# Kernel optimization log

Measured on AMD Instinct MI355X. Metric: run time of the kernel, lower is better.

Reference implementation:

```python
import jax, jax.numpy as jnp
import numpy as np

N = 50000
E = 800000
DIN = 128
DOUT = 128
T = 4  # number of edge types: onset, consecutive, during, rest


def setup_inputs() -> dict:
    key = jax.random.key(0)
    ks = jax.random.split(key, 12)
    s = 1.0 / np.sqrt(DIN)
    inp = {
        "x": jax.random.normal(ks[0], (N, DIN), dtype=jnp.float32),
        "edge_index": jax.random.randint(ks[1], (2, E), 0, N, dtype=jnp.int32),
        "edge_type": jax.random.randint(ks[2], (E,), 0, T, dtype=jnp.int32),
        # stacked per-etype parameters of ResGatedGraphConv
        "Wk": jax.random.uniform(ks[3], (T, DIN, DOUT), jnp.float32, -s, s),
        "bk": jax.random.uniform(ks[4], (T, DOUT), jnp.float32, -s, s),
        "Wq": jax.random.uniform(ks[5], (T, DIN, DOUT), jnp.float32, -s, s),
        "bq": jax.random.uniform(ks[6], (T, DOUT), jnp.float32, -s, s),
        "Wv": jax.random.uniform(ks[7], (T, DIN, DOUT), jnp.float32, -s, s),
        "bv": jax.random.uniform(ks[8], (T, DOUT), jnp.float32, -s, s),
        "Ws": jax.random.uniform(ks[9], (T, DIN, DOUT), jnp.float32, -s, s),
        "b": jax.random.uniform(ks[10], (T, DOUT), jnp.float32, -s, s),
    }
    return inp


def reference(x, edge_index, edge_type, Wk, bk, Wq, bq, Wv, bv, Ws, b):
    # PyG ResGatedGraphConv per edge type t, with edges masked to that type:
    #   out_i = sum_{j->i, type==t} sigmoid(k_i + q_j) * v_j + Ws_t x_i + b_t
    # followed by mean over edge types ('mean' reduction).
    src = edge_index[0]  # j (message source)
    dst = edge_index[1]  # i (message target)
    n = x.shape[0]
    outs = []
    for t in range(T):
        k = x @ Wk[t] + bk[t]  # [N, DOUT]
        q = x @ Wq[t] + bq[t]
        v = x @ Wv[t] + bv[t]
        eta = jax.nn.sigmoid(k[dst] + q[src])        # [E, DOUT]
        msg = eta * v[src]                            # [E, DOUT]
        msg = jnp.where((edge_type == t)[:, None], msg, 0.0)
        agg = jax.ops.segment_sum(msg, dst, num_segments=n)
        outs.append(agg + x @ Ws[t] + b[t])
    return jnp.mean(jnp.stack(outs, axis=0), axis=0)  # [N, DOUT]
```

## Files before the change

kernel.cpp:

```cpp
#include <hip/hip_runtime.h>

typedef unsigned short u16;
typedef unsigned int u32;
typedef __attribute__((ext_vector_type(8))) short bf16x8;
typedef __attribute__((ext_vector_type(4))) float f32x4;
typedef __attribute__((ext_vector_type(2))) float f32x2;
typedef __attribute__((ext_vector_type(8))) u16 u16x8;
typedef __attribute__((ext_vector_type(4))) u16 u16x4;
typedef __attribute__((ext_vector_type(2))) u16 u16x2;
typedef __attribute__((ext_vector_type(2))) u32 u32x2;

#define DIM 128
#define AS1C(p) ((const __attribute__((address_space(1))) void*)(p))
#define AS3P(p) ((__attribute__((address_space(3))) void*)(p))

__device__ __forceinline__ u32 f2bf(float f){
  u32 x = __float_as_uint(f);
  return (x + 0x7fffu + ((x >> 16) & 1u)) >> 16;
}
__device__ __forceinline__ float bf2f(u16 u){
  return __uint_as_float(((u32)u) << 16);
}

__global__ __launch_bounds__(256) void prep_kernel(
    const float* __restrict__ x, u16* __restrict__ xb,
    const float* __restrict__ Wk, const float* __restrict__ bk,
    const float* __restrict__ Wq, const float* __restrict__ bq,
    const float* __restrict__ Wv, const float* __restrict__ bv,
    const float* __restrict__ Ws, const float* __restrict__ bb,
    u16* __restrict__ WcatT, float* __restrict__ biascat,
    int* __restrict__ cnt, int T, int N, int rows){
  int id = blockIdx.x * 256 + threadIdx.x;
  int total_w = (3 * T + 1) * DIM * DIM;
  int total_cast = rows * (DIM / 4);
  if (id >= total_w){
    int z = id - total_w;
    if (z < total_cast){
      int el = z * 4;
      int node = el >> 7;
      u32x2 pk;
      if (node < N){
        f32x4 v = *(const f32x4*)(x + el);
        pk.x = f2bf(v.x) | (f2bf(v.y) << 16);
        pk.y = f2bf(v.z) | (f2bf(v.w) << 16);
      } else { pk.x = 0u; pk.y = 0u; }
      *(u32x2*)(xb + el) = pk;
    } else {
      int z2 = z - total_cast;
      if (z2 < N) cnt[z2] = 0;
    }
    return;
  }
  int kk = id & (DIM - 1);
  int c  = id >> 7;
  int qvspan = 2 * T * DIM;
  float wv, bvv;
  if (c < qvspan){
    int t = c >> 8;
    int w = c & 255;
    int j = w >> 1;
    if ((w & 1) == 0){ wv = Wq[(t*DIM + kk)*DIM + j]; bvv = bq[t*DIM + j]; }
    else             { wv = Wv[(t*DIM + kk)*DIM + j]; bvv = bv[t*DIM + j]; }
  } else if (c < qvspan + T * DIM){
    int t = (c - qvspan) >> 7;
    int j = (c - qvspan) & (DIM - 1);
    wv = Wk[(t*DIM + kk)*DIM + j]; bvv = bk[t*DIM + j];
  } else {
    int j = c - 3 * T * DIM;
    float s = 0.f, sb = 0.f;
    for (int t = 0; t < T; ++t){ s += Ws[(t*DIM + kk)*DIM + j]; sb += bb[t*DIM + j]; }
    wv = s / (float)T; bvv = sb / (float)T;
  }
  WcatT[(size_t)c * DIM + kk] = (u16)f2bf(wv);
  if (kk == 0) biascat[c] = bvv;
}

__global__ __launch_bounds__(256) void hist_kernel(const int* __restrict__ dst,
                                                   int* __restrict__ cnt,
                                                   int* __restrict__ rank, int E){
  int e = blockIdx.x * 256 + threadIdx.x;
  if (e < E) rank[e] = atomicAdd(&cnt[dst[e]], 1);
}

__global__ __launch_bounds__(256) void scan1_kernel(const int* __restrict__ cnt,
                                                    int* __restrict__ offs,
                                                    int* __restrict__ bsum, int n){
  __shared__ int wsum[4];
  const int tid = threadIdx.x;
  const int lane = tid & 63, wave = tid >> 6;
  const int base = blockIdx.x * 2048 + tid * 8;
  int v[8]; int tot = 0;
#pragma unroll
  for (int j = 0; j < 8; ++j){
    int idx = base + j;
    int val = (idx < n) ? cnt[idx] : 0;
    v[j] = val; tot += val;
  }
  int incl = tot;
#pragma unroll
  for (int d = 1; d < 64; d <<= 1){
    int u = __shfl_up(incl, d, 64);
    if (lane >= d) incl += u;
  }
  if (lane == 63) wsum[wave] = incl;
  __syncthreads();
  int wbase = 0;
#pragma unroll
  for (int w = 0; w < 4; ++w) if (w < wave) wbase += wsum[w];
  int excl = wbase + incl - tot;
  if (tid == 255) bsum[blockIdx.x] = wbase + incl;
#pragma unroll
  for (int j = 0; j < 8; ++j){
    int idx = base + j;
    if (idx < n) offs[idx] = excl;
    excl += v[j];
  }
}

__global__ __launch_bounds__(64) void scan2_kernel(const int* __restrict__ bsum,
                                                   int* __restrict__ boffs, int nb){
  int lane = threadIdx.x;
  int v = (lane < nb) ? bsum[lane] : 0;
  int incl = v;
#pragma unroll
  for (int d = 1; d < 64; d <<= 1){
    int u = __shfl_up(incl, d, 64);
    if (lane >= d) incl += u;
  }
  if (lane < nb) boffs[lane] = incl - v;
}

__global__ __launch_bounds__(256) void scatter_kernel(const int* __restrict__ src,
                                                      const int* __restrict__ dst,
                                                      const int* __restrict__ et,
                                                      const int* __restrict__ offs,
                                                      const int* __restrict__ boffs,
                                                      const int* __restrict__ rank,
                                                      int* __restrict__ packed, int E){
  int e = blockIdx.x * 256 + threadIdx.x;
  if (e >= E) return;
  int d = dst[e];
  int pos = offs[d] + boffs[d >> 11] + rank[e];
  packed[pos] = (src[e] << 2) | (et[e] & 3);
}

__global__ __launch_bounds__(256, 4) void gemm_kernel(const u16* __restrict__ xb,
                                                      const u16* __restrict__ WcatT,
                                                      const float* __restrict__ biascat,
                                                      u16* __restrict__ Y,
                                                      int N, int ncol, int NB, int mtiles){
  __shared__ u16 wt[DIM * DIM];
  int bid = blockIdx.x;
  int body = NB * (mtiles & ~7);
  int mt, nt;
  if (bid < body){
    int g = bid >> 3, r = bid & 7;
    int a = g / NB;
    mt = a * 8 + r;
    nt = g - a * NB;
  } else {
    int z = bid - body;
    mt = (mtiles & ~7) + z / NB;
    nt = z % NB;
  }
  const int m0 = mt * 128;
  const int n0 = nt * 128;
  const int tid  = threadIdx.x;
  const int wave = tid >> 6;
  const int lane = tid & 63;
  const int l15  = lane & 15;
  const int quad = lane >> 4;
  const int wrow = wave * 32;

  const u16* xrow0 = xb + (size_t)(m0 + wrow + l15) * DIM + quad * 8;
  const u16* xrow1 = xrow0 + 16 * DIM;

  bf16x8 bcur[2], bnxt[2];
  bcur[0] = *(const bf16x8*)(xrow0 + 0);
  bcur[1] = *(const bf16x8*)(xrow1 + 0);
  bnxt[0] = *(const bf16x8*)(xrow0 + 32);
  bnxt[1] = *(const bf16x8*)(xrow1 + 32);

#pragma unroll
  for (int it = 0; it < 8; ++it){
    int s  = it * 256 + tid;
    int r  = s >> 4;
    int p  = s & 15;
    int lb = p ^ (r & 7);
    int lbase = (it * 256 + wave * 64) * 8;
    __builtin_amdgcn_global_load_lds(AS1C(WcatT + (size_t)(n0 + r) * DIM + lb * 8),
                                     AS3P(wt + lbase), 16, 0, 0);
  }
  __syncthreads();

  f32x4 acc[2][8];
#pragma unroll
  for (int m = 0; m < 2; ++m)
#pragma unroll
    for (int f = 0; f < 8; ++f)
      acc[m][f] = (f32x4){0.f, 0.f, 0.f, 0.f};

#pragma unroll
  for (int ks = 0; ks < 4; ++ks){
    bf16x8 b0 = bcur[0], b1 = bcur[1];
    if (ks < 3){
      bcur[0] = bnxt[0]; bcur[1] = bnxt[1];
      if (ks < 2){
        bnxt[0] = *(const bf16x8*)(xrow0 + (ks + 2) * 32);
        bnxt[1] = *(const bf16x8*)(xrow1 + (ks + 2) * 32);
      }
    }
    const int pb8 = (((ks * 4 + quad) ^ (l15 & 7)) * 8);
#pragma unroll
    for (int f = 0; f < 8; ++f){
      bf16x8 afr = *(const bf16x8*)&wt[(f * 16 + l15) * DIM + pb8];
      acc[0][f] = __builtin_amdgcn_mfma_f32_16x16x32_bf16(afr, b0, acc[0][f], 0, 0, 0);
      acc[1][f] = __builtin_amdgcn_mfma_f32_16x16x32_bf16(afr, b1, acc[1][f], 0, 0, 0);
    }
  }

#pragma unroll
  for (int m = 0; m < 2; ++m){
    int node = m0 + wrow + m * 16 + l15;
    if (node >= N) continue;
    size_t rowbase = (size_t)node * ncol;
#pragma unroll
    for (int f = 0; f < 8; ++f){
      int feat = n0 + f * 16 + quad * 4;
      f32x4 b4 = *(const f32x4*)&biascat[feat];
      f32x4 v  = acc[m][f];
      u32 lo = f2bf(v.x + b4.x) | (f2bf(v.y + b4.y) << 16);
      u32 hi = f2bf(v.z + b4.z) | (f2bf(v.w + b4.w) << 16);
      u32x2 pk = {lo, hi};
      *(u32x2*)&Y[rowbase + feat] = pk;
    }
  }
}

__global__ __launch_bounds__(256) void agg_kernel(const u16* __restrict__ Y,
                                                  const int* __restrict__ offs,
                                                  const int* __restrict__ boffs,
                                                  const int* __restrict__ packed,
                                                  float* __restrict__ out,
                                                  int N, int E, float invT, int ncol){
  const int wave = threadIdx.x >> 6;
  const int lane = threadIdx.x & 63;
  const int half = lane >> 5;
  const int l32  = lane & 31;
  const int node = blockIdx.x * 8 + wave * 2 + half;
  const bool valid = node < N;
  const int nc = valid ? node : N - 1;

  const int kqoff = 1024;
  const int soff  = 1536;
  const u16* yr = Y + (size_t)nc * ncol;
  const int c4 = l32 * 4;

  u16x4 kw[4];
#pragma unroll
  for (int t = 0; t < 4; ++t)
    kw[t] = *(const u16x4*)(yr + kqoff + t * DIM + c4);
  u16x4 sw = *(const u16x4*)(yr + soff + c4);

  int e0 = 0, e1 = 0;
  if (valid){
    e0 = offs[nc] + boffs[nc >> 11];
    e1 = (nc == N - 1) ? E : (offs[nc + 1] + boffs[(nc + 1) >> 11]);
  }

  f32x4 acc = {0.f, 0.f, 0.f, 0.f};
  int e = e0;
  for (; e + 8 <= e1; e += 8){
    int p[8];
#pragma unroll
    for (int j = 0; j < 8; ++j) p[j] = packed[e + j];
    u16x8 a[8];
#pragma unroll
    for (int j = 0; j < 8; ++j)
      a[j] = *(const u16x8*)(Y + (size_t)(p[j] >> 2) * ncol + (p[j] & 3) * 256 + l32 * 8);
#pragma unroll
    for (int j = 0; j < 8; ++j){
      int t = p[j] & 3;
      u16x4 kwt = (t == 0) ? kw[0] : (t == 1) ? kw[1] : (t == 2) ? kw[2] : kw[3];
      acc.x += bf2f(a[j].s1) * __builtin_amdgcn_rcpf(1.f + __expf(-(bf2f(kwt.x) + bf2f(a[j].s0))));
      acc.y += bf2f(a[j].s3) * __builtin_amdgcn_rcpf(1.f + __expf(-(bf2f(kwt.y) + bf2f(a[j].s2))));
      acc.z += bf2f(a[j].s5) * __builtin_amdgcn_rcpf(1.f + __expf(-(bf2f(kwt.z) + bf2f(a[j].s4))));
      acc.w += bf2f(a[j].s7) * __builtin_amdgcn_rcpf(1.f + __expf(-(bf2f(kwt.w) + bf2f(a[j].s6))));
    }
  }
  for (; e < e1; ++e){
    int p = packed[e];
    int t = p & 3;
    u16x8 a = *(const u16x8*)(Y + (size_t)(p >> 2) * ncol + t * 256 + l32 * 8);
    u16x4 kwt = (t == 0) ? kw[0] : (t == 1) ? kw[1] : (t == 2) ? kw[2] : kw[3];
    acc.x += bf2f(a.s1) * __builtin_amdgcn_rcpf(1.f + __expf(-(bf2f(kwt.x) + bf2f(a.s0))));
    acc.y += bf2f(a.s3) * __builtin_amdgcn_rcpf(1.f + __expf(-(bf2f(kwt.y) + bf2f(a.s2))));
    acc.z += bf2f(a.s5) * __builtin_amdgcn_rcpf(1.f + __expf(-(bf2f(kwt.z) + bf2f(a.s4))));
    acc.w += bf2f(a.s7) * __builtin_amdgcn_rcpf(1.f + __expf(-(bf2f(kwt.w) + bf2f(a.s6))));
  }
  if (valid){
    f32x4 o = { invT * acc.x + bf2f(sw.x), invT * acc.y + bf2f(sw.y),
                invT * acc.z + bf2f(sw.z), invT * acc.w + bf2f(sw.w) };
    *(f32x4*)&out[(size_t)node * DIM + c4] = o;
  }
}

extern "C" void kernel_launch(void* const* d_in, const int* in_sizes, int n_in,
                              void* d_out, int out_size, void* d_ws, size_t ws_size,
                              hipStream_t stream){
  const float* x  = (const float*)d_in[0];
  const int*   ei = (const int*)d_in[1];
  const int*   et = (const int*)d_in[2];
  const float* Wk = (const float*)d_in[3];
  const float* bk = (const float*)d_in[4];
  const float* Wq = (const float*)d_in[5];
  const float* bq = (const float*)d_in[6];
  const float* Wv = (const float*)d_in[7];
  const float* bv = (const float*)d_in[8];
  const float* Ws = (const float*)d_in[9];
  const float* bb = (const float*)d_in[10];
  float* out = (float*)d_out;

  const int N = in_sizes[0] / DIM;
  const int E = in_sizes[2];
  const int T = in_sizes[3] / (DIM * DIM);
  const int NB = 3 * T + 1;
  const int ncol = NB * DIM;
  const int mtiles = (N + 127) / 128;
  const int rows = mtiles * 128;
  const int nscan = (N + 2047) / 2048;

  char* ws = (char*)d_ws;
  size_t off = 0;
  auto alloc = [&](size_t bytes) -> char* {
    char* p = ws + off;
    off = (off + bytes + 255) & ~(size_t)255;
    return p;
  };
  u16*   xb      = (u16*)alloc((size_t)rows * DIM * 2);
  u16*   WcatT   = (u16*)alloc((size_t)ncol * DIM * 2);
  float* biascat = (float*)alloc((size_t)ncol * 4);
  u16*   Y       = (u16*)alloc((size_t)N * ncol * 2);
  int*   cnt     = (int*)alloc((size_t)N * 4);
  int*   offs    = (int*)alloc((size_t)N * 4);
  int*   rank    = (int*)alloc((size_t)E * 4);
  int*   packed  = (int*)alloc((size_t)E * 4);
  int*   bsum    = (int*)alloc((size_t)nscan * 4);
  int*   boffs   = (int*)alloc((size_t)nscan * 4);
  (void)ws_size; (void)n_in; (void)out_size;

  const int* srcp = ei;
  const int* dstp = ei + E;

  int prep_total = NB * DIM * DIM + rows * (DIM / 4) + N;
  prep_kernel<<<(prep_total + 255) / 256, 256, 0, stream>>>(x, xb, Wk, bk, Wq, bq, Wv, bv,
                                                            Ws, bb, WcatT, biascat, cnt, T, N, rows);
  hist_kernel<<<(E + 255) / 256, 256, 0, stream>>>(dstp, cnt, rank, E);
  scan1_kernel<<<nscan, 256, 0, stream>>>(cnt, offs, bsum, N);
  scan2_kernel<<<1, 64, 0, stream>>>(bsum, boffs, nscan);
  scatter_kernel<<<(E + 255) / 256, 256, 0, stream>>>(srcp, dstp, et, offs, boffs, rank, packed, E);
  gemm_kernel<<<NB * mtiles, 256, 0, stream>>>(xb, WcatT, biascat, Y, N, ncol, NB, mtiles);
  agg_kernel<<<(N + 7) / 8, 256, 0, stream>>>(Y, offs, boffs, packed, out, N, E, 1.0f / (float)T, ncol);
}
```

Measured before the change: 306.1 us.

## Store q in fp8, repack Y rows, and fuse hist/scatter into prep and gemm

```diff
diff --git a/kernel.cpp b/kernel.cpp
--- a/kernel.cpp
+++ b/kernel.cpp
@@ -4,13 +4,15 @@
 typedef unsigned int u32;
 typedef __attribute__((ext_vector_type(8))) short bf16x8;
 typedef __attribute__((ext_vector_type(4))) float f32x4;
-typedef __attribute__((ext_vector_type(2))) float f32x2;
 typedef __attribute__((ext_vector_type(8))) u16 u16x8;
 typedef __attribute__((ext_vector_type(4))) u16 u16x4;
-typedef __attribute__((ext_vector_type(2))) u16 u16x2;
 typedef __attribute__((ext_vector_type(2))) u32 u32x2;
 
 #define DIM 128
+#define ROWB 2816
+#define QV_SPAN 384
+#define K_OFF 1536
+#define S_OFF 2560
 #define AS1C(p) ((const __attribute__((address_space(1))) void*)(p))
 #define AS3P(p) ((__attribute__((address_space(3))) void*)(p))
 
@@ -24,62 +26,51 @@
 
 __global__ __launch_bounds__(256) void prep_kernel(
     const float* __restrict__ x, u16* __restrict__ xb,
+    const int* __restrict__ dst, int* __restrict__ cnt, int* __restrict__ rank,
     const float* __restrict__ Wk, const float* __restrict__ bk,
     const float* __restrict__ Wq, const float* __restrict__ bq,
     const float* __restrict__ Wv, const float* __restrict__ bv,
     const float* __restrict__ Ws, const float* __restrict__ bb,
     u16* __restrict__ WcatT, float* __restrict__ biascat,
-    int* __restrict__ cnt, int T, int N, int rows){
+    int T, int N, int E, int rows){
   int id = blockIdx.x * 256 + threadIdx.x;
+  if (id < E){
+    rank[id] = atomicAdd(&cnt[dst[id]], 1);
+    return;
+  }
+  id -= E;
   int total_w = (3 * T + 1) * DIM * DIM;
+  if (id < total_w){
+    int kk = id & (DIM - 1);
+    int c  = id >> 7;
+    int nt = c >> 7;
+    int j  = c & (DIM - 1);
+    float wv, bvv;
+    if (nt < T)          { wv = Wq[(nt*DIM + kk)*DIM + j];      bvv = bq[nt*DIM + j]; }
+    else if (nt < 2*T)   { wv = Wv[((nt-T)*DIM + kk)*DIM + j];  bvv = bv[(nt-T)*DIM + j]; }
+    else if (nt < 3*T)   { wv = Wk[((nt-2*T)*DIM + kk)*DIM + j];bvv = bk[(nt-2*T)*DIM + j]; }
+    else {
+      float s = 0.f, sb = 0.f;
+      for (int t = 0; t < T; ++t){ s += Ws[(t*DIM + kk)*DIM + j]; sb += bb[t*DIM + j]; }
+      wv = s / (float)T; bvv = sb / (float)T;
+    }
+    WcatT[(size_t)c * DIM + kk] = (u16)f2bf(wv);
+    if (kk == 0) biascat[c] = bvv;
+    return;
+  }
+  id -= total_w;
   int total_cast = rows * (DIM / 4);
-  if (id >= total_w){
-    int z = id - total_w;
-    if (z < total_cast){
-      int el = z * 4;
-      int node = el >> 7;
-      u32x2 pk;
-      if (node < N){
-        f32x4 v = *(const f32x4*)(x + el);
-        pk.x = f2bf(v.x) | (f2bf(v.y) << 16);
-        pk.y = f2bf(v.z) | (f2bf(v.w) << 16);
-      } else { pk.x = 0u; pk.y = 0u; }
-      *(u32x2*)(xb + el) = pk;
-    } else {
-      int z2 = z - total_cast;
-      if (z2 < N) cnt[z2] = 0;
-    }
-    return;
-  }
-  int kk = id & (DIM - 1);
-  int c  = id >> 7;
-  int qvspan = 2 * T * DIM;
-  float wv, bvv;
-  if (c < qvspan){
-    int t = c >> 8;
-    int w = c & 255;
-    int j = w >> 1;
-    if ((w & 1) == 0){ wv = Wq[(t*DIM + kk)*DIM + j]; bvv = bq[t*DIM + j]; }
-    else             { wv = Wv[(t*DIM + kk)*DIM + j]; bvv = bv[t*DIM + j]; }
-  } else if (c < qvspan + T * DIM){
-    int t = (c - qvspan) >> 7;
-    int j = (c - qvspan) & (DIM - 1);
-    wv = Wk[(t*DIM + kk)*DIM + j]; bvv = bk[t*DIM + j];
-  } else {
-    int j = c - 3 * T * DIM;
-    float s = 0.f, sb = 0.f;
-    for (int t = 0; t < T; ++t){ s += Ws[(t*DIM + kk)*DIM + j]; sb += bb[t*DIM + j]; }
-    wv = s / (float)T; bvv = sb / (float)T;
-  }
-  WcatT[(size_t)c * DIM + kk] = (u16)f2bf(wv);
-  if (kk == 0) biascat[c] = bvv;
-}
-
-__global__ __launch_bounds__(256) void hist_kernel(const int* __restrict__ dst,
-                                                   int* __restrict__ cnt,
-                                                   int* __restrict__ rank, int E){
-  int e = blockIdx.x * 256 + threadIdx.x;
-  if (e < E) rank[e] = atomicAdd(&cnt[dst[e]], 1);
+  if (id < total_cast){
+    int el = id * 4;
+    int node = el >> 7;
+    u32x2 pk;
+    if (node < N){
+      f32x4 v = *(const f32x4*)(x + el);
+      pk.x = f2bf(v.x) | (f2bf(v.y) << 16);
+      pk.y = f2bf(v.z) | (f2bf(v.w) << 16);
+    } else { pk.x = 0u; pk.y = 0u; }
+    *(u32x2*)(xb + el) = pk;
+  }
 }
 
 __global__ __launch_bounds__(256) void scan1_kernel(const int* __restrict__ cnt,
@@ -130,27 +121,26 @@
   if (lane < nb) boffs[lane] = incl - v;
 }
 
-__global__ __launch_bounds__(256) void scatter_kernel(const int* __restrict__ src,
-                                                      const int* __restrict__ dst,
-                                                      const int* __restrict__ et,
-                                                      const int* __restrict__ offs,
-                                                      const int* __restrict__ boffs,
-                                                      const int* __restrict__ rank,
-                                                      int* __restrict__ packed, int E){
-  int e = blockIdx.x * 256 + threadIdx.x;
-  if (e >= E) return;
-  int d = dst[e];
-  int pos = offs[d] + boffs[d >> 11] + rank[e];
-  packed[pos] = (src[e] << 2) | (et[e] & 3);
-}
-
-__global__ __launch_bounds__(256, 4) void gemm_kernel(const u16* __restrict__ xb,
-                                                      const u16* __restrict__ WcatT,
-                                                      const float* __restrict__ biascat,
-                                                      u16* __restrict__ Y,
-                                                      int N, int ncol, int NB, int mtiles){
+__global__ __launch_bounds__(256, 4) void gemm_scatter_kernel(
+    const u16* __restrict__ xb, const u16* __restrict__ WcatT,
+    const float* __restrict__ biascat, char* __restrict__ Y,
+    const int* __restrict__ src, const int* __restrict__ dst,
+    const int* __restrict__ et, const int* __restrict__ offs,
+    const int* __restrict__ boffs, const int* __restrict__ rank,
+    int* __restrict__ packed,
+    int N, int E, int T, int NB, int mtiles, int nsc){
   __shared__ u16 wt[DIM * DIM];
   int bid = blockIdx.x;
+  if (bid < nsc){
+    int e = bid * 256 + threadIdx.x;
+    if (e < E){
+      int d = dst[e];
+      int pos = offs[d] + boffs[d >> 11] + rank[e];
+      packed[pos] = (src[e] << 2) | (et[e] & 3);
+    }
+    return;
+  }
+  bid -= nsc;
   int body = NB * (mtiles & ~7);
   int mt, nt;
   if (bid < body){
@@ -223,26 +213,37 @@
   for (int m = 0; m < 2; ++m){
     int node = m0 + wrow + m * 16 + l15;
     if (node >= N) continue;
-    size_t rowbase = (size_t)node * ncol;
+    char* rb = Y + (size_t)node * ROWB;
 #pragma unroll
     for (int f = 0; f < 8; ++f){
-      int feat = n0 + f * 16 + quad * 4;
-      f32x4 b4 = *(const f32x4*)&biascat[feat];
+      int feat = f * 16 + quad * 4;
+      f32x4 b4 = *(const f32x4*)&biascat[n0 + feat];
       f32x4 v  = acc[m][f];
-      u32 lo = f2bf(v.x + b4.x) | (f2bf(v.y + b4.y) << 16);
-      u32 hi = f2bf(v.z + b4.z) | (f2bf(v.w + b4.w) << 16);
-      u32x2 pk = {lo, hi};
-      *(u32x2*)&Y[rowbase + feat] = pk;
-    }
-  }
-}
-
-__global__ __launch_bounds__(256) void agg_kernel(const u16* __restrict__ Y,
+      float a0 = v.x + b4.x, a1 = v.y + b4.y, a2 = v.z + b4.z, a3 = v.w + b4.w;
+      if (nt < T){
+        u32 w = __builtin_amdgcn_cvt_pk_fp8_f32(a0, a1, 0, false);
+        w = __builtin_amdgcn_cvt_pk_fp8_f32(a2, a3, w, true);
+        *(u32*)(rb + nt * QV_SPAN + feat) = w;
+      } else {
+        u32 lo = f2bf(a0) | (f2bf(a1) << 16);
+        u32 hi = f2bf(a2) | (f2bf(a3) << 16);
+        u32x2 pk = {lo, hi};
+        int boff;
+        if (nt < 2*T)      boff = (nt - T) * QV_SPAN + 128;
+        else if (nt < 3*T) boff = K_OFF + (nt - 2*T) * 256;
+        else               boff = S_OFF;
+        *(u32x2*)(rb + boff + feat * 2) = pk;
+      }
+    }
+  }
+}
+
+__global__ __launch_bounds__(256) void agg_kernel(const char* __restrict__ Y,
                                                   const int* __restrict__ offs,
                                                   const int* __restrict__ boffs,
                                                   const int* __restrict__ packed,
                                                   float* __restrict__ out,
-                                                  int N, int E, float invT, int ncol){
+                                                  int N, int E, float invT){
   const int wave = threadIdx.x >> 6;
   const int lane = threadIdx.x & 63;
   const int half = lane >> 5;
@@ -251,16 +252,15 @@
   const bool valid = node < N;
   const int nc = valid ? node : N - 1;
 
-  const int kqoff = 1024;
-  const int soff  = 1536;
-  const u16* yr = Y + (size_t)nc * ncol;
-  const int c4 = l32 * 4;
-
-  u16x4 kw[4];
-#pragma unroll
-  for (int t = 0; t < 4; ++t)
-    kw[t] = *(const u16x4*)(yr + kqoff + t * DIM + c4);
-  u16x4 sw = *(const u16x4*)(yr + soff + c4);
+  const char* yr = Y + (size_t)nc * ROWB;
+
+  f32x4 kf[4];
+#pragma unroll
+  for (int t = 0; t < 4; ++t){
+    u16x4 kw = *(const u16x4*)(yr + K_OFF + t * 256 + l32 * 8);
+    kf[t] = (f32x4){ bf2f(kw.x), bf2f(kw.y), bf2f(kw.z), bf2f(kw.w) };
+  }
+  u16x4 sw = *(const u16x4*)(yr + S_OFF + l32 * 8);
 
   int e0 = 0, e1 = 0;
   if (valid){
@@ -274,34 +274,39 @@
     int p[8];
 #pragma unroll
     for (int j = 0; j < 8; ++j) p[j] = packed[e + j];
-    u16x8 a[8];
-#pragma unroll
-    for (int j = 0; j < 8; ++j)
-      a[j] = *(const u16x8*)(Y + (size_t)(p[j] >> 2) * ncol + (p[j] & 3) * 256 + l32 * 8);
+    u32 qw[8]; u16x4 vw[8];
+#pragma unroll
+    for (int j = 0; j < 8; ++j){
+      const char* sb = Y + (size_t)(p[j] >> 2) * ROWB + (p[j] & 3) * QV_SPAN;
+      qw[j] = *(const u32*)(sb + l32 * 4);
+      vw[j] = *(const u16x4*)(sb + 128 + l32 * 8);
+    }
 #pragma unroll
     for (int j = 0; j < 8; ++j){
       int t = p[j] & 3;
-      u16x4 kwt = (t == 0) ? kw[0] : (t == 1) ? kw[1] : (t == 2) ? kw[2] : kw[3];
-      acc.x += bf2f(a[j].s1) * __builtin_amdgcn_rcpf(1.f + __expf(-(bf2f(kwt.x) + bf2f(a[j].s0))));
-      acc.y += bf2f(a[j].s3) * __builtin_amdgcn_rcpf(1.f + __expf(-(bf2f(kwt.y) + bf2f(a[j].s2))));
-      acc.z += bf2f(a[j].s5) * __builtin_amdgcn_rcpf(1.f + __expf(-(bf2f(kwt.z) + bf2f(a[j].s4))));
-      acc.w += bf2f(a[j].s7) * __builtin_amdgcn_rcpf(1.f + __expf(-(bf2f(kwt.w) + bf2f(a[j].s6))));
+      f32x4 kt = (t == 0) ? kf[0] : (t == 1) ? kf[1] : (t == 2) ? kf[2] : kf[3];
+      acc.x += bf2f(vw[j].x) * __builtin_amdgcn_rcpf(1.f + __expf(-(kt.x + __builtin_amdgcn_cvt_f32_fp8(qw[j], 0))));
+      acc.y += bf2f(vw[j].y) * __builtin_amdgcn_rcpf(1.f + __expf(-(kt.y + __builtin_amdgcn_cvt_f32_fp8(qw[j], 1))));
+      acc.z += bf2f(vw[j].z) * __builtin_amdgcn_rcpf(1.f + __expf(-(kt.z + __builtin_amdgcn_cvt_f32_fp8(qw[j], 2))));
+      acc.w += bf2f(vw[j].w) * __builtin_amdgcn_rcpf(1.f + __expf(-(kt.w + __builtin_amdgcn_cvt_f32_fp8(qw[j], 3))));
     }
   }
   for (; e < e1; ++e){
     int p = packed[e];
     int t = p & 3;
-    u16x8 a = *(const u16x8*)(Y + (size_t)(p >> 2) * ncol + t * 256 + l32 * 8);
-    u16x4 kwt = (t == 0) ? kw[0] : (t == 1) ? kw[1] : (t == 2) ? kw[2] : kw[3];
-    acc.x += bf2f(a.s1) * __builtin_amdgcn_rcpf(1.f + __expf(-(bf2f(kwt.x) + bf2f(a.s0))));
-    acc.y += bf2f(a.s3) * __builtin_amdgcn_rcpf(1.f + __expf(-(bf2f(kwt.y) + bf2f(a.s2))));
-    acc.z += bf2f(a.s5) * __builtin_amdgcn_rcpf(1.f + __expf(-(bf2f(kwt.z) + bf2f(a.s4))));
-    acc.w += bf2f(a.s7) * __builtin_amdgcn_rcpf(1.f + __expf(-(bf2f(kwt.w) + bf2f(a.s6))));
+    const char* sb = Y + (size_t)(p >> 2) * ROWB + t * QV_SPAN;
+    u32 qw = *(const u32*)(sb + l32 * 4);
+    u16x4 vw = *(const u16x4*)(sb + 128 + l32 * 8);
+    f32x4 kt = (t == 0) ? kf[0] : (t == 1) ? kf[1] : (t == 2) ? kf[2] : kf[3];
+    acc.x += bf2f(vw.x) * __builtin_amdgcn_rcpf(1.f + __expf(-(kt.x + __builtin_amdgcn_cvt_f32_fp8(qw, 0))));
+    acc.y += bf2f(vw.y) * __builtin_amdgcn_rcpf(1.f + __expf(-(kt.y + __builtin_amdgcn_cvt_f32_fp8(qw, 1))));
+    acc.z += bf2f(vw.z) * __builtin_amdgcn_rcpf(1.f + __expf(-(kt.z + __builtin_amdgcn_cvt_f32_fp8(qw, 2))));
+    acc.w += bf2f(vw.w) * __builtin_amdgcn_rcpf(1.f + __expf(-(kt.w + __builtin_amdgcn_cvt_f32_fp8(qw, 3))));
   }
   if (valid){
     f32x4 o = { invT * acc.x + bf2f(sw.x), invT * acc.y + bf2f(sw.y),
                 invT * acc.z + bf2f(sw.z), invT * acc.w + bf2f(sw.w) };
-    *(f32x4*)&out[(size_t)node * DIM + c4] = o;
+    *(f32x4*)&out[(size_t)node * DIM + l32 * 4] = o;
   }
 }
 
@@ -329,6 +334,7 @@
   const int mtiles = (N + 127) / 128;
   const int rows = mtiles * 128;
   const int nscan = (N + 2047) / 2048;
+  const int nsc = (E + 255) / 256;
 
   char* ws = (char*)d_ws;
   size_t off = 0;
@@ -340,7 +346,7 @@
   u16*   xb      = (u16*)alloc((size_t)rows * DIM * 2);
   u16*   WcatT   = (u16*)alloc((size_t)ncol * DIM * 2);
   float* biascat = (float*)alloc((size_t)ncol * 4);
-  u16*   Y       = (u16*)alloc((size_t)N * ncol * 2);
+  char*  Y       = (char*)alloc((size_t)rows * ROWB);
   int*   cnt     = (int*)alloc((size_t)N * 4);
   int*   offs    = (int*)alloc((size_t)N * 4);
   int*   rank    = (int*)alloc((size_t)E * 4);
@@ -352,13 +358,15 @@
   const int* srcp = ei;
   const int* dstp = ei + E;
 
-  int prep_total = NB * DIM * DIM + rows * (DIM / 4) + N;
-  prep_kernel<<<(prep_total + 255) / 256, 256, 0, stream>>>(x, xb, Wk, bk, Wq, bq, Wv, bv,
-                                                            Ws, bb, WcatT, biascat, cnt, T, N, rows);
-  hist_kernel<<<(E + 255) / 256, 256, 0, stream>>>(dstp, cnt, rank, E);
+  hipMemsetAsync(cnt, 0, (size_t)N * 4, stream);
+  int prep_total = E + NB * DIM * DIM + rows * (DIM / 4);
+  prep_kernel<<<(prep_total + 255) / 256, 256, 0, stream>>>(
+      x, xb, dstp, cnt, rank, Wk, bk, Wq, bq, Wv, bv, Ws, bb,
+      WcatT, biascat, T, N, E, rows);
   scan1_kernel<<<nscan, 256, 0, stream>>>(cnt, offs, bsum, N);
   scan2_kernel<<<1, 64, 0, stream>>>(bsum, boffs, nscan);
-  scatter_kernel<<<(E + 255) / 256, 256, 0, stream>>>(srcp, dstp, et, offs, boffs, rank, packed, E);
-  gemm_kernel<<<NB * mtiles, 256, 0, stream>>>(xb, WcatT, biascat, Y, N, ncol, NB, mtiles);
-  agg_kernel<<<(N + 7) / 8, 256, 0, stream>>>(Y, offs, boffs, packed, out, N, E, 1.0f / (float)T, ncol);
-}
+  gemm_scatter_kernel<<<nsc + NB * mtiles, 256, 0, stream>>>(
+      xb, WcatT, biascat, Y, srcp, dstp, et, offs, boffs, rank, packed,
+      N, E, T, NB, mtiles, nsc);
+  agg_kernel<<<(N + 7) / 8, 256, 0, stream>>>(Y, offs, boffs, packed, out, N, E, 1.0f / (float)T);
+}
```

New measurement: 289.7 us. -5.4%, faster.
